# Optimization experiments

Hardware: AMD Instinct MI355X
Metric: run time of the kernel (lower is better)

Reference implementation:

```python
import jax, jax.numpy as jnp
import numpy as np

D_MODEL = 1024
HEADS = 16
D_K = D_MODEL // HEADS
THETA = 10000.0
NEG = -1.0e9


def _rope(t, offset=0):
    # t: [B, H, S, D]; standard interleaved rotary embedding, base THETA
    S, D = t.shape[-2], t.shape[-1]
    half = D // 2
    inv_freq = 1.0 / (THETA ** (jnp.arange(half, dtype=jnp.float32) * 2.0 / D))
    pos = jnp.arange(offset, offset + S, dtype=jnp.float32)
    ang = pos[:, None] * inv_freq[None, :]          # [S, half]
    cos, sin = jnp.cos(ang), jnp.sin(ang)
    t1, t2 = t[..., ::2], t[..., 1::2]              # even / odd lanes
    o1 = t1 * cos - t2 * sin
    o2 = t1 * sin + t2 * cos
    return jnp.stack([o1, o2], axis=-1).reshape(t.shape)


def setup_inputs() -> dict:
    key = jax.random.key(0)
    k0, k1, k2, k3, k4 = jax.random.split(key, 5)
    B, S = 2, 2048
    x = jax.random.normal(k0, (B, S, D_MODEL), dtype=jnp.float32)
    att_mask = jnp.ones((B, S), dtype=jnp.int32)
    scale = 0.02
    wq = jax.random.normal(k1, (D_MODEL, D_MODEL), dtype=jnp.float32) * scale
    wk = jax.random.normal(k2, (D_MODEL, D_MODEL), dtype=jnp.float32) * scale
    wv = jax.random.normal(k3, (D_MODEL, D_MODEL), dtype=jnp.float32) * scale
    wo = jax.random.normal(k4, (D_MODEL, D_MODEL), dtype=jnp.float32) * scale
    return {"x": x, "att_mask": att_mask, "wq": wq, "wk": wk, "wv": wv, "wo": wo}


def reference(x, att_mask, wq, wk, wv, wo):
    B, S, _ = x.shape
    # nn.Linear(bias=False): y = x @ W^T ; then split heads -> [B, H, S, d_k]
    q = (x @ wq.T).reshape(B, S, HEADS, D_K).transpose(0, 2, 1, 3)
    k = (x @ wk.T).reshape(B, S, HEADS, D_K).transpose(0, 2, 1, 3)
    v = (x @ wv.T).reshape(B, S, HEADS, D_K).transpose(0, 2, 1, 3)
    # use_rope=True, start_pos=0, use_cache=False path
    q = _rope(q)
    k = _rope(k)
    scores = jnp.einsum("bhqd,bhkd->bhqk", q, k) / np.sqrt(D_K).astype(np.float32)
    pad = (att_mask == 0)[:, None, None, :]          # [B,1,1,S]
    scores = jnp.where(pad, NEG, scores)
    causal = jnp.tril(jnp.ones((S, S), dtype=bool))  # [S, S]
    scores = jnp.where(causal, scores, NEG)
    att = jax.nn.softmax(scores, axis=-1)
    ctx = jnp.einsum("bhqk,bhkd->bhqd", att, v)      # [B,H,S,d_k]
    final = ctx.transpose(0, 2, 1, 3).reshape(B, S, HEADS * D_K)
    return final @ wo.T
```

## Files before the change

### kernel.cpp

```cpp
#include <hip/hip_runtime.h>
#include <hip/hip_bf16.h>
#include <cstdint>

typedef unsigned short u16;
typedef __bf16 bf16x8 __attribute__((ext_vector_type(8)));
typedef float f32x4 __attribute__((ext_vector_type(4)));

#define S_LEN 2048
#define NH 16
#define DK 64
#define DM 1024

__device__ __forceinline__ u16 f2bf(float f) {
  union { float f; uint32_t u; } c; c.f = f;
  uint32_t u = c.u;
  u += 0x7fffu + ((u >> 16) & 1u);
  return (u16)(u >> 16);
}

__device__ __forceinline__ void gl_lds16(const void* gsrc, void* ldst) {
  __builtin_amdgcn_global_load_lds(
      (const __attribute__((address_space(1))) unsigned int*)gsrc,
      (__attribute__((address_space(3))) unsigned int*)ldst,
      16, 0, 0);
}

#define MFMA16(a, b, c) __builtin_amdgcn_mfma_f32_16x16x32_bf16((a), (b), (c), 0, 0, 0)
#define VMW(N) asm volatile("s_waitcnt vmcnt(" #N ")" ::: "memory")
#define BARM() asm volatile("s_barrier" ::: "memory")

__global__ __launch_bounds__(256) void prep_all(
    const float* x, const float* wq, const float* wk, const float* wv, const float* wo,
    const int* amask,
    u16* xb, u16* wqb, u16* wkb, u16* wvb, u16* wob, float2* tab, int* mflag)
{
  const int bid = blockIdx.x;
  if (bid < 2048) {
#pragma unroll
    for (int it = 0; it < 4; ++it) {
      size_t i = ((size_t)bid * 256 + threadIdx.x) * 4 + (size_t)it * 2097152u;
      const float* src; u16* dst; size_t off;
      if (i < 4194304u)      { src = x;  dst = xb;  off = i; }
      else if (i < 5242880u) { src = wq; dst = wqb; off = i - 4194304u; }
      else if (i < 6291456u) { src = wk; dst = wkb; off = i - 5242880u; }
      else if (i < 7340032u) { src = wv; dst = wvb; off = i - 6291456u; }
      else                   { src = wo; dst = wob; off = i - 7340032u; }
      float4 v = *(const float4*)(src + off);
      ushort4 o;
      o.x = f2bf(v.x); o.y = f2bf(v.y); o.z = f2bf(v.z); o.w = f2bf(v.w);
      *(ushort4*)(dst + off) = o;
    }
  } else if (bid < 2304) {
    int i = (bid - 2048) * 256 + threadIdx.x;
    int pos = i >> 5, f = i & 31;
    float inv = powf(10000.0f, -(float)f / 32.0f);
    float ang = (float)pos * inv;
    tab[i] = make_float2(cosf(ang), sinf(ang));
  } else {
    const int f = bid - 2304;
    if (threadIdx.x < 64) {
      const int b = f >> 5, t = f & 31;
      int v = amask[b * S_LEN + t * 64 + threadIdx.x];
      int all = (int)__all(v != 0);
      if (threadIdx.x == 0) mflag[f] = all;
    }
  }
}

__global__ __launch_bounds__(256) void gemm_qkv128(
    const u16* xb, const u16* wqb, const u16* wkb, const u16* wvb,
    const float2* tab, u16* Qr, u16* Kr, u16* Vt)
{
  __shared__ __align__(16) u16 ldsA[2][128 * 64];
  __shared__ __align__(16) u16 ldsB[2][128 * 64];

  const int bid = blockIdx.x;
  const int xcd = bid & 7, v = bid >> 3;
  const int m0 = (xcd * 4 + (v & 3)) * 128;
  const int nc = v >> 2;
  const int z = nc >> 3;
  const int n0z = (nc & 7) * 128;
  const u16* Wz = (z == 0) ? wqb : ((z == 1) ? wkb : wvb);

  const int tid = threadIdx.x;
  const int w = tid >> 6, lane = tid & 63;
  const int l15 = lane & 15, g = lane >> 4;
  const int wm = (w >> 1) * 64, wn = (w & 1) * 64;
  const int lrow = lane >> 3;
  const int scolb = ((lane & 7) * 16) ^ (lrow << 4);
  f32x4 acc[4][4] = {};

  auto stage = [&](int buf, int kt) {
#pragma unroll
    for (int c = 0; c < 4; ++c) {
      const int rb = w * 32 + c * 8;
      const int row = rb + lrow;
      gl_lds16((const char*)(xb + (size_t)(m0 + row) * DM + kt) + scolb,
               (char*)&ldsA[buf][0] + rb * 128);
      gl_lds16((const char*)(Wz + (size_t)(n0z + row) * DM + kt) + scolb,
               (char*)&ldsB[buf][0] + rb * 128);
    }
  };

  stage(0, 0);
  int cur = 0;
  for (int kt = 0; kt < DM; kt += 64) {
    if (kt + 64 < DM) { stage(cur ^ 1, kt + 64); VMW(8); } else { VMW(0); }
    BARM();
#pragma unroll
    for (int ks = 0; ks < 2; ++ks) {
      bf16x8 af[4], bfr[4];
#pragma unroll
      for (int i = 0; i < 4; ++i) {
        const int ar = wm + i * 16 + l15;
        af[i] = *(const bf16x8*)((const char*)&ldsA[cur][0] + ar * 128 +
                                 ((ks * 64 + g * 16) ^ ((ar & 7) << 4)));
        const int br = wn + i * 16 + l15;
        bfr[i] = *(const bf16x8*)((const char*)&ldsB[cur][0] + br * 128 +
                                  ((ks * 64 + g * 16) ^ ((br & 7) << 4)));
      }
      __builtin_amdgcn_s_setprio(1);
#pragma unroll
      for (int i = 0; i < 4; ++i)
#pragma unroll
        for (int j = 0; j < 4; ++j)
          acc[i][j] = MFMA16(af[i], bfr[j], acc[i][j]);
      __builtin_amdgcn_s_setprio(0);
    }
    BARM();
    cur ^= 1;
  }

  u16* dst = (z == 0) ? Qr : Kr;
#pragma unroll
  for (int i = 0; i < 4; ++i) {
#pragma unroll
    for (int j = 0; j < 4; ++j) {
      const int n = n0z + wn + j * 16 + l15;
      const int h = n >> 6, d = n & 63;
#pragma unroll
      for (int r = 0; r < 4; ++r) {
        const int m = m0 + wm + i * 16 + g * 4 + r;
        const int b = m >> 11, s = m & 2047;
        float vv = acc[i][j][r];
        if (z < 2) {
          float p = __shfl_xor(vv, 1);
          float2 cs = tab[s * 32 + (d >> 1)];
          float o = vv * cs.x + ((d & 1) ? p : -p) * cs.y;
          if (z == 0) o *= 0.18033688011f;
          dst[((size_t)(b * NH + h) * S_LEN + s) * DK + d] = f2bf(o);
        } else {
          Vt[((size_t)(b * NH + h) * DK + d) * S_LEN + s] = f2bf(vv);
        }
      }
    }
  }
}

__device__ __forceinline__ void xcd_map(int bid, int& m0, int& n0) {
  const int xcd = bid & 7, v = bid >> 3;
  m0 = (xcd * 4 + (v >> 3)) * 128;
  n0 = (v & 7) * 128;
}

__global__ __launch_bounds__(256) void gemm_out(const u16* ctx, const u16* wob, float* out) {
  __shared__ __align__(16) u16 ldsA[2][128 * 64];
  __shared__ __align__(16) u16 ldsB[2][128 * 64];
  int m0, n0;
  xcd_map(blockIdx.x, m0, n0);

  const int tid = threadIdx.x;
  const int w = tid >> 6, lane = tid & 63;
  const int l15 = lane & 15, g = lane >> 4;
  const int wm = (w >> 1) * 64, wn = (w & 1) * 64;
  const int lrow = lane >> 3;
  const int scolb = ((lane & 7) * 16) ^ (lrow << 4);
  f32x4 acc[4][4] = {};

  auto stage = [&](int buf, int kt) {
#pragma unroll
    for (int c = 0; c < 4; ++c) {
      const int rb = w * 32 + c * 8;
      const int row = rb + lrow;
      gl_lds16((const char*)(ctx + (size_t)(m0 + row) * DM + kt) + scolb,
               (char*)&ldsA[buf][0] + rb * 128);
      gl_lds16((const char*)(wob + (size_t)(n0 + row) * DM + kt) + scolb,
               (char*)&ldsB[buf][0] + rb * 128);
    }
  };

  stage(0, 0);
  int cur = 0;
  for (int kt = 0; kt < DM; kt += 64) {
    if (kt + 64 < DM) { stage(cur ^ 1, kt + 64); VMW(8); } else { VMW(0); }
    BARM();
#pragma unroll
    for (int ks = 0; ks < 2; ++ks) {
      bf16x8 af[4], bfr[4];
#pragma unroll
      for (int i = 0; i < 4; ++i) {
        const int ar = wm + i * 16 + l15;
        af[i] = *(const bf16x8*)((const char*)&ldsA[cur][0] + ar * 128 +
                                 ((ks * 64 + g * 16) ^ ((ar & 7) << 4)));
        const int br = wn + i * 16 + l15;
        bfr[i] = *(const bf16x8*)((const char*)&ldsB[cur][0] + br * 128 +
                                  ((ks * 64 + g * 16) ^ ((br & 7) << 4)));
      }
      __builtin_amdgcn_s_setprio(1);
#pragma unroll
      for (int i = 0; i < 4; ++i)
#pragma unroll
        for (int j = 0; j < 4; ++j)
          acc[i][j] = MFMA16(af[i], bfr[j], acc[i][j]);
      __builtin_amdgcn_s_setprio(0);
    }
    BARM();
    cur ^= 1;
  }

#pragma unroll
  for (int i = 0; i < 4; ++i)
#pragma unroll
    for (int j = 0; j < 4; ++j)
#pragma unroll
      for (int r = 0; r < 4; ++r)
        out[(size_t)(m0 + wm + i * 16 + g * 4 + r) * DM + n0 + wn + j * 16 + l15] = acc[i][j][r];
}

__global__ __launch_bounds__(512, 4) void attn11(
    const u16* Qr, const u16* Kr, const u16* Vt, const int* amask, const int* mflag,
    u16* ctx)
{
  __shared__ __align__(16) u16 ldsK[2][64 * 64];
  __shared__ __align__(16) u16 ldsV[2][64 * 64];
  __shared__ __align__(16) __bf16 plds[8][16 * 72];

  const int bh = blockIdx.x;
  const int by = blockIdx.y;
  const int band = (by < 8) ? (15 - by) : (by - 8);
  const int b = bh >> 4, h = bh & 15;
  const int tid = threadIdx.x, w8 = tid >> 6, lane = tid & 63;
  const int l15 = lane & 15, g = lane >> 4;
  const int r8 = lane >> 3;
  const int sw = ((lane & 7) * 16) ^ (r8 << 4);

  const int chunk = band * 4 + (w8 >> 1);
  const int q0 = chunk * 32 + (w8 & 1) * 16;
  const int myNt = (chunk >> 1) + 1;
  const int dTile = chunk >> 1;
  const int ntB = band * 2 + 2;

  const u16* Kb0 = Kr + (size_t)bh * S_LEN * DK;
  const u16* Vb0 = Vt + (size_t)bh * DK * S_LEN;
  const u16* Qb  = Qr + (size_t)bh * S_LEN * DK;

  bf16x8 qa0 = *(const bf16x8*)(Qb + (size_t)(q0 + l15) * DK + g * 8);
  bf16x8 qa1 = *(const bf16x8*)(Qb + (size_t)(q0 + l15) * DK + 32 + g * 8);

  union { u16 u[8]; bf16x8 v; } one_u;
#pragma unroll
  for (int i = 0; i < 8; ++i) one_u.u[i] = 0x3F80;
  const bf16x8 ones = one_u.v;

  float m[4];
  f32x4 lacc = {0.f, 0.f, 0.f, 0.f};
  f32x4 o[4];
#pragma unroll
  for (int r = 0; r < 4; ++r) m[r] = -3e38f;
#pragma unroll
  for (int dt = 0; dt < 4; ++dt) o[dt] = (f32x4){0.f, 0.f, 0.f, 0.f};

  auto stage = [&](int buf, int t) {
    const size_t kv0 = (size_t)t * 64;
    const int row = w8 * 8 + r8;
    gl_lds16((const char*)(Kb0 + (kv0 + row) * DK) + sw,
             (char*)&ldsK[buf][0] + (w8 * 8) * 128);
    gl_lds16((const char*)(Vb0 + (size_t)row * S_LEN + kv0) + sw,
             (char*)&ldsV[buf][0] + (w8 * 8) * 128);
  };

  stage(0, 0);
  int cur = 0;

  for (int t = 0; t < ntB; ++t) {
    if (t + 1 < ntB) { stage(cur ^ 1, t + 1); VMW(2); } else { VMW(0); }
    BARM();
    if (t < myNt) {
      const int kv0 = t * 64;
      const bool allok = mflag[(b << 5) + t] != 0;

      bf16x8 kb[4][2];
#pragma unroll
      for (int nt = 0; nt < 4; ++nt) {
        const int row = nt * 16 + l15;
#pragma unroll
        for (int ks = 0; ks < 2; ++ks)
          kb[nt][ks] = *(const bf16x8*)((const char*)&ldsK[cur][0] + row * 128 +
                                        ((ks * 64 + g * 16) ^ ((row & 7) << 4)));
      }
      f32x4 s[4];
#pragma unroll
      for (int nt = 0; nt < 4; ++nt) s[nt] = (f32x4){0.f, 0.f, 0.f, 0.f};
      __builtin_amdgcn_s_setprio(1);
#pragma unroll
      for (int nt = 0; nt < 4; ++nt) {
        s[nt] = MFMA16(qa0, kb[nt][0], s[nt]);
        s[nt] = MFMA16(qa1, kb[nt][1], s[nt]);
      }
      __builtin_amdgcn_s_setprio(0);

      if (!allok) {
#pragma unroll
        for (int nt = 0; nt < 4; ++nt) {
          const int pmv = amask[b * S_LEN + kv0 + nt * 16 + l15];
#pragma unroll
          for (int r = 0; r < 4; ++r)
            if (!pmv) s[nt][r] = -1e9f;
        }
      }
      if (t == dTile) {
#pragma unroll
        for (int nt = 0; nt < 4; ++nt) {
          const int kvc = kv0 + nt * 16 + l15;
#pragma unroll
          for (int r = 0; r < 4; ++r)
            s[nt][r] = (kvc <= q0 + g * 4 + r) ? s[nt][r] : -1e9f;
        }
      }

      float tmax[4];
      bool need = false;
#pragma unroll
      for (int r = 0; r < 4; ++r) {
        float t0 = fmaxf(fmaxf(s[0][r], s[1][r]), fmaxf(s[2][r], s[3][r]));
        t0 = fmaxf(t0, __shfl_xor(t0, 1));
        t0 = fmaxf(t0, __shfl_xor(t0, 2));
        t0 = fmaxf(t0, __shfl_xor(t0, 4));
        t0 = fmaxf(t0, __shfl_xor(t0, 8));
        tmax[r] = t0;
        need = need || (t0 > m[r] + 11.5415603f);
      }
      if (__any((int)need)) {
#pragma unroll
        for (int r = 0; r < 4; ++r) {
          const float mnew = fmaxf(m[r], tmax[r]);
          const float alpha = exp2f(m[r] - mnew);
          m[r] = mnew;
          lacc[r] *= alpha;
#pragma unroll
          for (int dt = 0; dt < 4; ++dt) o[dt][r] *= alpha;
        }
      }
      __bf16* pw = &plds[w8][0];
#pragma unroll
      for (int r = 0; r < 4; ++r) {
#pragma unroll
        for (int nt = 0; nt < 4; ++nt)
          pw[(g * 4 + r) * 72 + nt * 16 + l15] = (__bf16)exp2f(s[nt][r] - m[r]);
      }
      bf16x8 pa0 = *(const bf16x8*)(pw + l15 * 72 + g * 8);
      bf16x8 pa1 = *(const bf16x8*)(pw + l15 * 72 + 32 + g * 8);
      bf16x8 vb[4][2];
#pragma unroll
      for (int dt = 0; dt < 4; ++dt) {
        const int row = dt * 16 + l15;
#pragma unroll
        for (int ks = 0; ks < 2; ++ks)
          vb[dt][ks] = *(const bf16x8*)((const char*)&ldsV[cur][0] + row * 128 +
                                        ((ks * 64 + g * 16) ^ ((row & 7) << 4)));
      }
      __builtin_amdgcn_s_setprio(1);
      lacc = MFMA16(pa0, ones, lacc);
      lacc = MFMA16(pa1, ones, lacc);
#pragma unroll
      for (int dt = 0; dt < 4; ++dt) {
        o[dt] = MFMA16(pa0, vb[dt][0], o[dt]);
        o[dt] = MFMA16(pa1, vb[dt][1], o[dt]);
      }
      __builtin_amdgcn_s_setprio(0);
    }
    BARM();
    cur ^= 1;
  }

#pragma unroll
  for (int dt = 0; dt < 4; ++dt)
#pragma unroll
    for (int r = 0; r < 4; ++r) {
      const int q = q0 + g * 4 + r;
      ctx[((size_t)(b * S_LEN + q)) * DM + h * DK + dt * 16 + l15] =
          f2bf(o[dt][r] / lacc[r]);
    }
}

extern "C" void kernel_launch(void* const* d_in, const int* in_sizes, int n_in,
                              void* d_out, int out_size, void* d_ws, size_t ws_size,
                              hipStream_t stream) {
  const float* x   = (const float*)d_in[0];
  const int* amask = (const int*)d_in[1];
  const float* wq  = (const float*)d_in[2];
  const float* wk  = (const float*)d_in[3];
  const float* wv  = (const float*)d_in[4];
  const float* wo  = (const float*)d_in[5];
  float* out = (float*)d_out;

  char* ws = (char*)d_ws;
  u16* xb    = (u16*)(ws);
  u16* wqb   = (u16*)(ws + ( 8u << 20));
  u16* wkb   = (u16*)(ws + (10u << 20));
  u16* wvb   = (u16*)(ws + (12u << 20));
  u16* wob   = (u16*)(ws + (14u << 20));
  float2* tab = (float2*)(ws + (16u << 20));
  int* mflag = (int*)(ws + (16u << 20) + (768u << 10));
  u16* Qr    = (u16*)(ws + (17u << 20));
  u16* Kr    = (u16*)(ws + (25u << 20));
  u16* Vt    = (u16*)(ws + (33u << 20));
  u16* ctx   = (u16*)(ws + (41u << 20));

  hipLaunchKernelGGL(prep_all, dim3(2368), dim3(256), 0, stream,
                     x, wq, wk, wv, wo, amask, xb, wqb, wkb, wvb, wob, tab, mflag);
  hipLaunchKernelGGL(gemm_qkv128, dim3(768), dim3(256), 0, stream,
                     xb, wqb, wkb, wvb, tab, Qr, Kr, Vt);
  hipLaunchKernelGGL(attn11, dim3(32, 16), dim3(512), 0, stream,
                     Qr, Kr, Vt, amask, mflag, ctx);
  hipLaunchKernelGGL(gemm_out, dim3(256), dim3(256), 0, stream, ctx, wob, out);
}
```

Baseline: 153.5 us.

## Halve GEMM K-tile to 32 and split output GEMM into 128x64 tiles

The QKV projection GEMM now stages 32-wide K slices instead of 64, halving LDS per block and adding an occupancy hint of 4 blocks per CU. The output projection GEMM moves to 128x64 tiles with 512 blocks, so the grid covers more of the GPU's compute units, and it also uses 32-wide K slices. The cost is twice as many loop iterations and barriers per tile, and a smaller MFMA-to-load ratio in the output GEMM.

```diff
diff --git a/kernel.cpp b/kernel.cpp
--- a/kernel.cpp
+++ b/kernel.cpp
@@ -67,12 +67,12 @@
   }
 }
 
-__global__ __launch_bounds__(256) void gemm_qkv128(
+__global__ __launch_bounds__(256, 4) void gemm_qkv32(
     const u16* xb, const u16* wqb, const u16* wkb, const u16* wvb,
     const float2* tab, u16* Qr, u16* Kr, u16* Vt)
 {
-  __shared__ __align__(16) u16 ldsA[2][128 * 64];
-  __shared__ __align__(16) u16 ldsB[2][128 * 64];
+  __shared__ __align__(16) u16 ldsA[2][128 * 32];
+  __shared__ __align__(16) u16 ldsB[2][128 * 32];
 
   const int bid = blockIdx.x;
   const int xcd = bid & 7, v = bid >> 3;
@@ -86,47 +86,45 @@
   const int w = tid >> 6, lane = tid & 63;
   const int l15 = lane & 15, g = lane >> 4;
   const int wm = (w >> 1) * 64, wn = (w & 1) * 64;
-  const int lrow = lane >> 3;
-  const int scolb = ((lane & 7) * 16) ^ (lrow << 4);
+  const int lr4 = lane >> 2;
+  const int scolb = ((lane & 3) * 16) ^ ((lr4 & 3) << 4);
+
   f32x4 acc[4][4] = {};
 
   auto stage = [&](int buf, int kt) {
 #pragma unroll
-    for (int c = 0; c < 4; ++c) {
-      const int rb = w * 32 + c * 8;
-      const int row = rb + lrow;
+    for (int c = 0; c < 2; ++c) {
+      const int rb = c * 64 + w * 16;
+      const int row = rb + lr4;
       gl_lds16((const char*)(xb + (size_t)(m0 + row) * DM + kt) + scolb,
-               (char*)&ldsA[buf][0] + rb * 128);
+               (char*)&ldsA[buf][0] + rb * 64);
       gl_lds16((const char*)(Wz + (size_t)(n0z + row) * DM + kt) + scolb,
-               (char*)&ldsB[buf][0] + rb * 128);
+               (char*)&ldsB[buf][0] + rb * 64);
     }
   };
 
   stage(0, 0);
   int cur = 0;
-  for (int kt = 0; kt < DM; kt += 64) {
-    if (kt + 64 < DM) { stage(cur ^ 1, kt + 64); VMW(8); } else { VMW(0); }
-    BARM();
-#pragma unroll
-    for (int ks = 0; ks < 2; ++ks) {
-      bf16x8 af[4], bfr[4];
-#pragma unroll
-      for (int i = 0; i < 4; ++i) {
-        const int ar = wm + i * 16 + l15;
-        af[i] = *(const bf16x8*)((const char*)&ldsA[cur][0] + ar * 128 +
-                                 ((ks * 64 + g * 16) ^ ((ar & 7) << 4)));
-        const int br = wn + i * 16 + l15;
-        bfr[i] = *(const bf16x8*)((const char*)&ldsB[cur][0] + br * 128 +
-                                  ((ks * 64 + g * 16) ^ ((br & 7) << 4)));
-      }
-      __builtin_amdgcn_s_setprio(1);
-#pragma unroll
-      for (int i = 0; i < 4; ++i)
-#pragma unroll
-        for (int j = 0; j < 4; ++j)
-          acc[i][j] = MFMA16(af[i], bfr[j], acc[i][j]);
-      __builtin_amdgcn_s_setprio(0);
-    }
+  for (int kt = 0; kt < DM; kt += 32) {
+    if (kt + 32 < DM) { stage(cur ^ 1, kt + 32); VMW(4); } else { VMW(0); }
+    BARM();
+    bf16x8 af[4], bfr[4];
+#pragma unroll
+    for (int i = 0; i < 4; ++i) {
+      const int ar = wm + i * 16 + l15;
+      af[i] = *(const bf16x8*)((const char*)&ldsA[cur][0] + ar * 64 +
+                               ((g * 16) ^ ((ar & 3) << 4)));
+      const int br = wn + i * 16 + l15;
+      bfr[i] = *(const bf16x8*)((const char*)&ldsB[cur][0] + br * 64 +
+                                ((g * 16) ^ ((br & 3) << 4)));
+    }
+    __builtin_amdgcn_s_setprio(1);
+#pragma unroll
+    for (int i = 0; i < 4; ++i)
+#pragma unroll
+      for (int j = 0; j < 4; ++j)
+        acc[i][j] = MFMA16(af[i], bfr[j], acc[i][j]);
+    __builtin_amdgcn_s_setprio(0);
     BARM();
     cur ^= 1;
   }
@@ -157,63 +155,63 @@
   }
 }
 
-__device__ __forceinline__ void xcd_map(int bid, int& m0, int& n0) {
+__global__ __launch_bounds__(256, 4) void gemm_out64(const u16* ctx, const u16* wob, float* out) {
+  __shared__ __align__(16) u16 ldsA[2][128 * 32];
+  __shared__ __align__(16) u16 ldsB[2][64 * 32];
+
+  const int bid = blockIdx.x;
   const int xcd = bid & 7, v = bid >> 3;
-  m0 = (xcd * 4 + (v >> 3)) * 128;
-  n0 = (v & 7) * 128;
-}
-
-__global__ __launch_bounds__(256) void gemm_out(const u16* ctx, const u16* wob, float* out) {
-  __shared__ __align__(16) u16 ldsA[2][128 * 64];
-  __shared__ __align__(16) u16 ldsB[2][128 * 64];
-  int m0, n0;
-  xcd_map(blockIdx.x, m0, n0);
+  const int m0 = (xcd * 4 + (v & 3)) * 128;
+  const int n0 = (v >> 2) * 64;
 
   const int tid = threadIdx.x;
   const int w = tid >> 6, lane = tid & 63;
   const int l15 = lane & 15, g = lane >> 4;
-  const int wm = (w >> 1) * 64, wn = (w & 1) * 64;
-  const int lrow = lane >> 3;
-  const int scolb = ((lane & 7) * 16) ^ (lrow << 4);
-  f32x4 acc[4][4] = {};
+  const int wm = (w >> 1) * 64, wn = (w & 1) * 32;
+  const int lr4 = lane >> 2;
+  const int scolb = ((lane & 3) * 16) ^ ((lr4 & 3) << 4);
+
+  f32x4 acc[4][2] = {};
 
   auto stage = [&](int buf, int kt) {
 #pragma unroll
-    for (int c = 0; c < 4; ++c) {
-      const int rb = w * 32 + c * 8;
-      const int row = rb + lrow;
+    for (int c = 0; c < 2; ++c) {
+      const int rb = c * 64 + w * 16;
+      const int row = rb + lr4;
       gl_lds16((const char*)(ctx + (size_t)(m0 + row) * DM + kt) + scolb,
-               (char*)&ldsA[buf][0] + rb * 128);
-      gl_lds16((const char*)(wob + (size_t)(n0 + row) * DM + kt) + scolb,
-               (char*)&ldsB[buf][0] + rb * 128);
-    }
+               (char*)&ldsA[buf][0] + rb * 64);
+    }
+    const int rb = w * 16;
+    const int row = rb + lr4;
+    gl_lds16((const char*)(wob + (size_t)(n0 + row) * DM + kt) + scolb,
+             (char*)&ldsB[buf][0] + rb * 64);
   };
 
   stage(0, 0);
   int cur = 0;
-  for (int kt = 0; kt < DM; kt += 64) {
-    if (kt + 64 < DM) { stage(cur ^ 1, kt + 64); VMW(8); } else { VMW(0); }
-    BARM();
-#pragma unroll
-    for (int ks = 0; ks < 2; ++ks) {
-      bf16x8 af[4], bfr[4];
-#pragma unroll
-      for (int i = 0; i < 4; ++i) {
-        const int ar = wm + i * 16 + l15;
-        af[i] = *(const bf16x8*)((const char*)&ldsA[cur][0] + ar * 128 +
-                                 ((ks * 64 + g * 16) ^ ((ar & 7) << 4)));
-        const int br = wn + i * 16 + l15;
-        bfr[i] = *(const bf16x8*)((const char*)&ldsB[cur][0] + br * 128 +
-                                  ((ks * 64 + g * 16) ^ ((br & 7) << 4)));
-      }
-      __builtin_amdgcn_s_setprio(1);
-#pragma unroll
-      for (int i = 0; i < 4; ++i)
-#pragma unroll
-        for (int j = 0; j < 4; ++j)
-          acc[i][j] = MFMA16(af[i], bfr[j], acc[i][j]);
-      __builtin_amdgcn_s_setprio(0);
-    }
+  for (int kt = 0; kt < DM; kt += 32) {
+    if (kt + 32 < DM) { stage(cur ^ 1, kt + 32); VMW(3); } else { VMW(0); }
+    BARM();
+    bf16x8 af[4], bfr[2];
+#pragma unroll
+    for (int i = 0; i < 4; ++i) {
+      const int ar = wm + i * 16 + l15;
+      af[i] = *(const bf16x8*)((const char*)&ldsA[cur][0] + ar * 64 +
+                               ((g * 16) ^ ((ar & 3) << 4)));
+    }
+#pragma unroll
+    for (int j = 0; j < 2; ++j) {
+      const int br = wn + j * 16 + l15;
+      bfr[j] = *(const bf16x8*)((const char*)&ldsB[cur][0] + br * 64 +
+                                ((g * 16) ^ ((br & 3) << 4)));
+    }
+    __builtin_amdgcn_s_setprio(1);
+#pragma unroll
+    for (int i = 0; i < 4; ++i)
+#pragma unroll
+      for (int j = 0; j < 2; ++j)
+        acc[i][j] = MFMA16(af[i], bfr[j], acc[i][j]);
+    __builtin_amdgcn_s_setprio(0);
     BARM();
     cur ^= 1;
   }
@@ -221,7 +219,7 @@
 #pragma unroll
   for (int i = 0; i < 4; ++i)
 #pragma unroll
-    for (int j = 0; j < 4; ++j)
+    for (int j = 0; j < 2; ++j)
 #pragma unroll
       for (int r = 0; r < 4; ++r)
         out[(size_t)(m0 + wm + i * 16 + g * 4 + r) * DM + n0 + wn + j * 16 + l15] = acc[i][j][r];
@@ -419,9 +417,9 @@
 
   hipLaunchKernelGGL(prep_all, dim3(2368), dim3(256), 0, stream,
                      x, wq, wk, wv, wo, amask, xb, wqb, wkb, wvb, wob, tab, mflag);
-  hipLaunchKernelGGL(gemm_qkv128, dim3(768), dim3(256), 0, stream,
+  hipLaunchKernelGGL(gemm_qkv32, dim3(768), dim3(256), 0, stream,
                      xb, wqb, wkb, wvb, tab, Qr, Kr, Vt);
   hipLaunchKernelGGL(attn11, dim3(32, 16), dim3(512), 0, stream,
                      Qr, Kr, Vt, amask, mflag, ctx);
-  hipLaunchKernelGGL(gemm_out, dim3(256), dim3(256), 0, stream, ctx, wob, out);
-}
+  hipLaunchKernelGGL(gemm_out64, dim3(512), dim3(256), 0, stream, ctx, wob, out);
+}
```

Result: faster. 144.2 us (-6.0%).
